# Kernel tuning notes

Measured on AMD Instinct MI355X. Metric: run time of the kernel, lower is better.

## Reference

```python
import jax, jax.numpy as jnp
import numpy as np

B, N, D, H = 2, 2048, 1024, 16
DH = D // H            # 64
PH = 3 * DH            # 192 per-head proj dim (module quirk: 3*Dh per head)
P = H * PH             # 3072 total projection width


def setup_inputs() -> dict:
    key = jax.random.key(0)
    ks = jax.random.split(key, 8)
    s = 0.02
    return {
        "input": jax.random.normal(ks[0], (B, N, D), dtype=jnp.float32),
        "q_w": jax.random.normal(ks[1], (D, P), dtype=jnp.float32) * s,
        "q_b": jnp.zeros((P,), dtype=jnp.float32),
        "k_w": jax.random.normal(ks[2], (D, P), dtype=jnp.float32) * s,
        "k_b": jnp.zeros((P,), dtype=jnp.float32),
        "v_w": jax.random.normal(ks[3], (D, P), dtype=jnp.float32) * s,
        "v_b": jnp.zeros((P,), dtype=jnp.float32),
        "o_w": jax.random.normal(ks[4], (P, D), dtype=jnp.float32) * s,
        "o_b": jnp.zeros((D,), dtype=jnp.float32),
    }


def reference(input, q_w, q_b, k_w, k_b, v_w, v_b, o_w, o_b):
    def heads(y):  # [B,N,H*PH] -> [B,H,N,PH]
        return y.reshape(B, N, H, PH).transpose(0, 2, 1, 3)

    q_mat = heads(input @ q_w + q_b)
    # faithful to source: v_mat uses the 'k' projection, k_mat uses the 'v' projection
    v_mat = heads(input @ k_w + k_b)
    k_mat = heads(input @ v_w + v_b)

    scale = 1.0 / jnp.sqrt(jnp.float32(DH * H))  # sqrt(dim), per source
    scores = jnp.einsum('bhnd,bhmd->bhnm', q_mat, k_mat) * scale
    weights = jax.nn.softmax(scores, axis=-1)
    inter = jnp.einsum('bhnm,bhmd->bhnd', weights, v_mat)
    inter = inter.transpose(0, 2, 1, 3).reshape(B, N, P)  # b n (h d)
    return inter @ o_w + o_b
```

## Files before the change

kernel.cpp:

```cpp
#include <hip/hip_runtime.h>
#include <cstdint>
#include <cstddef>

typedef __bf16 bf16;
typedef __attribute__((ext_vector_type(8))) __bf16 bf16x8;
typedef __attribute__((ext_vector_type(4))) __bf16 bf16x4;
typedef __attribute__((ext_vector_type(2))) __bf16 bf16x2;
typedef __attribute__((ext_vector_type(4))) float f32x4;

#define MFMA_16x16x32(a, b, c) __builtin_amdgcn_mfma_f32_16x16x32_bf16((a), (b), (c), 0, 0, 0)

#define VMCNT(N) asm volatile("s_waitcnt vmcnt(" #N ")" ::: "memory")
#define LGK0                                           \
  {                                                    \
    asm volatile("s_waitcnt lgkmcnt(0)" ::: "memory"); \
    __builtin_amdgcn_sched_barrier(0);                 \
  }

__device__ __forceinline__ void gload_lds16(const void* g, void* l) {
  __builtin_amdgcn_global_load_lds((__attribute__((address_space(1))) void*)g,
                                   (__attribute__((address_space(3))) void*)l,
                                   16, 0, 0);
}

__global__ __launch_bounds__(256) void prep_kernel(const float* __restrict__ X,
                                                   const float* __restrict__ q_w,
                                                   const float* __restrict__ v_w,
                                                   const float* __restrict__ k_w,
                                                   const float* __restrict__ o_w,
                                                   bf16* __restrict__ Xb,
                                                   bf16* __restrict__ Wqkv,
                                                   bf16* __restrict__ Wot) {
  __shared__ float tile[32][33];
  int blk = blockIdx.x;
  if (blk < 4096) {
    int i = blk * 256 + threadIdx.x;
    float4 v = ((const float4*)X)[i];
    bf16x4 o = {(bf16)v.x, (bf16)v.y, (bf16)v.z, (bf16)v.w};
    ((bf16x4*)Xb)[i] = o;
    return;
  }
  const float* in;
  bf16* out;
  int R, C, t;
  if (blk < 13312) {
    t = blk - 4096;
    int widx = t / 3072;
    t -= widx * 3072;
    in = widx == 0 ? q_w : (widx == 1 ? v_w : k_w);
    out = Wqkv + (size_t)widx * 3072 * 1024;
    R = 1024;
    C = 3072;
  } else {
    t = blk - 13312;
    in = o_w;
    out = Wot;
    R = 3072;
    C = 1024;
  }
  int tiles_c = C >> 5;
  int br = t / tiles_c, bc = t % tiles_c;
  int r0 = br << 5, c0 = bc << 5;
  int tr = threadIdx.x >> 5, tc = threadIdx.x & 31;
#pragma unroll
  for (int i = 0; i < 4; i++)
    tile[tr + 8 * i][tc] = in[(size_t)(r0 + tr + 8 * i) * C + c0 + tc];
  __syncthreads();
#pragma unroll
  for (int i = 0; i < 4; i++) {
    int oc = tr + 8 * i;
    out[(size_t)(c0 + oc) * R + r0 + tc] = (bf16)tile[tc][oc];
  }
}

__global__ __launch_bounds__(512, 2) void gemm_fused_qkv(
    const bf16* __restrict__ A, const bf16* __restrict__ Bt,
    const float* __restrict__ q_b, const float* __restrict__ v_b,
    const float* __restrict__ k_b,
    bf16* __restrict__ Qm, bf16* __restrict__ Km, bf16* __restrict__ Vt) {
  constexpr int K = 1024, NT = 16;
  __shared__ __align__(16) bf16 sA[2][2][128 * 32];
  __shared__ __align__(16) bf16 sB[2][192 * 64];

  int bid = blockIdx.x;
  int xcd = bid & 7, j = bid >> 3;
  int bm = xcd * 4 + (j & 3), bn = j >> 2;
  int m0 = bm << 7, n0 = bn * 192;

  int tid = threadIdx.x, lane = tid & 63, w = tid >> 6;
  int wr = w >> 2, wc = w & 3;
  int l15 = lane & 15, lg = lane >> 4;

  int sra = lane >> 2, sca = lane & 3;
  const bf16* gA = A + (size_t)(m0 + w * 16 + sra) * K + ((sca ^ ((sra >> 1) & 3)) * 8);
  int srb = lane >> 3, scb = lane & 7;
  const bf16* gB = Bt + (size_t)(n0 + w * 24 + srb) * K + ((scb ^ srb) * 8);

#define STAGE_AB(BUF, T)                                                   \
  {                                                                        \
    _Pragma("unroll") for (int kh = 0; kh < 2; kh++)                       \
        gload_lds16(gA + (size_t)(T) * 64 + kh * 32, &sA[BUF][kh][w * 512]); \
    _Pragma("unroll") for (int ii = 0; ii < 3; ii++)                       \
        gload_lds16(gB + (size_t)(ii * 8) * K + (T) * 64,                  \
                    &sB[BUF][(w * 3 + ii) * 512]);                         \
  }

  int slotA = lg ^ ((l15 >> 1) & 3);
  int aBase = wr * 2048 + l15 * 32 + slotA * 8;
  int bBase = (wc * 48 + l15) * 64;
  int sB0 = (lg ^ (l15 & 7)) * 8;
  int sB1 = ((4 + lg) ^ (l15 & 7)) * 8;

#define RD_A(BUF, KH)                                                      \
  _Pragma("unroll") for (int mf = 0; mf < 4; mf++)                         \
      a[mf] = *(const bf16x8*)&sA[BUF][KH][aBase + mf * 512];
#define RD_B(BUF, SLOT)                                                    \
  _Pragma("unroll") for (int nf = 0; nf < 3; nf++)                         \
      b[nf] = *(const bf16x8*)&sB[BUF][bBase + nf * 1024 + (SLOT)];
#define MFMA12                                                             \
  _Pragma("unroll") for (int mf = 0; mf < 4; mf++)                         \
      _Pragma("unroll") for (int nf = 0; nf < 3; nf++)                     \
          acc[mf][nf] = MFMA_16x16x32(a[mf], b[nf], acc[mf][nf]);

  f32x4 acc[4][3];
#pragma unroll
  for (int mf = 0; mf < 4; mf++)
#pragma unroll
    for (int nf = 0; nf < 3; nf++) acc[mf][nf] = (f32x4){0.f, 0.f, 0.f, 0.f};

  STAGE_AB(0, 0);

#pragma unroll 2
  for (int s = 0; s < NT; s++) {
    int buf = s & 1, nbuf = buf ^ 1;
    int nxt = (s + 1) & (NT - 1);
    bf16x8 a[4], b[3];

    STAGE_AB(nbuf, nxt);
    VMCNT(5);
    __builtin_amdgcn_s_barrier();

    RD_A(buf, 0);
    RD_B(buf, sB0);
    LGK0;
    __builtin_amdgcn_s_setprio(1);
    MFMA12;
    __builtin_amdgcn_s_setprio(0);

    RD_A(buf, 1);
    RD_B(buf, sB1);
    LGK0;
    __builtin_amdgcn_s_barrier();
    __builtin_amdgcn_s_setprio(1);
    MFMA12;
    __builtin_amdgcn_s_setprio(0);
  }

  int seg = bn >> 4;
  int segbn = bn & 15;
  const float* bias = seg == 0 ? q_b : (seg == 1 ? v_b : k_b);
  bf16* outQK = seg == 0 ? Qm : Km;
#pragma unroll
  for (int mf = 0; mf < 4; mf++) {
#pragma unroll
    for (int nf = 0; nf < 3; nf++) {
      int colL = segbn * 192 + wc * 48 + nf * 16 + l15;
      int row0 = m0 + wr * 64 + mf * 16 + lg * 4;
      float bv = bias[colL];
      if (seg < 2) {
#pragma unroll
        for (int r = 0; r < 4; r++)
          outQK[(size_t)(row0 + r) * 3072 + colL] = (bf16)(acc[mf][nf][r] + bv);
      } else {
        int hh = colL / 192, dd = colL % 192;
        int bi = row0 >> 11, nn = row0 & 2047;
        bf16x4 pk = {(bf16)(acc[mf][nf][0] + bv), (bf16)(acc[mf][nf][1] + bv),
                     (bf16)(acc[mf][nf][2] + bv), (bf16)(acc[mf][nf][3] + bv)};
        *(bf16x4*)(Vt + (((size_t)bi * 16 + hh) * 192 + dd) * 2048 + nn) = pk;
      }
    }
  }
#undef STAGE_AB
#undef RD_A
#undef RD_B
#undef MFMA12
}

__global__ __launch_bounds__(256, 3) void gemm_oproj(const bf16* __restrict__ A,
                                                     const bf16* __restrict__ Bt,
                                                     const float* __restrict__ bias,
                                                     float* __restrict__ out) {
  constexpr int K = 3072, NT = 48;
  __shared__ __align__(16) bf16 sA[2][2][128 * 32];
  __shared__ __align__(16) bf16 sB[2][2][64 * 32];

  int bid = blockIdx.x;
  int xcd = bid & 7, j = bid >> 3;
  int bm = xcd * 4 + (j & 3), bn = j >> 2;
  int m0 = bm << 7, n0 = bn << 6;

  int tid = threadIdx.x, lane = tid & 63, w = tid >> 6;
  int wr = w >> 1, wc = w & 1;
  int l15 = lane & 15, lg = lane >> 4;

  int sra = lane >> 2, sca = lane & 3;
  int swzS = (sca ^ ((sra >> 1) & 3)) * 8;
  const bf16* gA = A + (size_t)(m0 + w * 32 + sra) * K + swzS;
  const bf16* gB = Bt + (size_t)(n0 + w * 16 + sra) * K + swzS;

#define O_STAGE(BUF, T)                                                     \
  {                                                                         \
    _Pragma("unroll") for (int kh = 0; kh < 2; kh++) {                      \
      _Pragma("unroll") for (int ii = 0; ii < 2; ii++)                      \
          gload_lds16(gA + (size_t)(ii * 16) * K + (T) * 64 + kh * 32,      \
                      &sA[BUF][kh][(w * 32 + ii * 16) * 32]);               \
      gload_lds16(gB + (size_t)(T) * 64 + kh * 32, &sB[BUF][kh][w * 512]);  \
    }                                                                       \
  }

  int slotA = lg ^ ((l15 >> 1) & 3);
  int aBase = (wr * 64 + l15) * 32 + slotA * 8;
  int bBase = (wc * 32 + l15) * 32 + slotA * 8;

#define O_RD(BUF, KH)                                                      \
  {                                                                        \
    _Pragma("unroll") for (int mf = 0; mf < 4; mf++)                       \
        a[mf] = *(const bf16x8*)&sA[BUF][KH][aBase + mf * 512];             \
    _Pragma("unroll") for (int nf = 0; nf < 2; nf++)                       \
        b[nf] = *(const bf16x8*)&sB[BUF][KH][bBase + nf * 512];             \
  }
#define O_MFMA8                                                            \
  _Pragma("unroll") for (int mf = 0; mf < 4; mf++)                         \
      _Pragma("unroll") for (int nf = 0; nf < 2; nf++)                     \
          acc[mf][nf] = MFMA_16x16x32(a[mf], b[nf], acc[mf][nf]);

  f32x4 acc[4][2];
#pragma unroll
  for (int mf = 0; mf < 4; mf++)
#pragma unroll
    for (int nf = 0; nf < 2; nf++) acc[mf][nf] = (f32x4){0.f, 0.f, 0.f, 0.f};

  O_STAGE(0, 0);

#pragma unroll 2
  for (int s = 0; s < NT; s++) {
    int buf = s & 1, nbuf = buf ^ 1;
    int nxt = s + 1 < NT ? s + 1 : 0;
    bf16x8 a[4], b[2];

    O_STAGE(nbuf, nxt);
    VMCNT(6);
    __builtin_amdgcn_s_barrier();

    O_RD(buf, 0);
    LGK0;
    __builtin_amdgcn_s_setprio(1);
    O_MFMA8;
    __builtin_amdgcn_s_setprio(0);

    O_RD(buf, 1);
    LGK0;
    __builtin_amdgcn_s_barrier();
    __builtin_amdgcn_s_setprio(1);
    O_MFMA8;
    __builtin_amdgcn_s_setprio(0);
  }

#pragma unroll
  for (int mf = 0; mf < 4; mf++) {
#pragma unroll
    for (int nf = 0; nf < 2; nf++) {
      int col = n0 + wc * 32 + nf * 16 + l15;
      int row0 = m0 + wr * 64 + mf * 16 + lg * 4;
      float bv = bias[col];
#pragma unroll
      for (int r = 0; r < 4; r++)
        out[(size_t)(row0 + r) * 1024 + col] = acc[mf][nf][r] + bv;
    }
  }
#undef O_STAGE
#undef O_RD
#undef O_MFMA8
}

__global__ __launch_bounds__(512, 2) void attn_kernel(const bf16* __restrict__ Q,
                                                      const bf16* __restrict__ Km,
                                                      const bf16* __restrict__ Vt,
                                                      bf16* __restrict__ inter) {
  __shared__ __align__(16) bf16 sK[2][64 * 192];
  __shared__ __align__(16) bf16 sV[2][192 * 64];
  __shared__ __align__(16) bf16 sPT[8 * 2 * 16 * 72];

  int i = blockIdx.x;
  int j = i >> 3;
  int bh = (i & 7) * 4 + (j >> 3);
  int qt = j & 7;
  int b = bh >> 4, h = bh & 15;
  int tid = threadIdx.x, lane = tid & 63, w = tid >> 6;
  int l15 = lane & 15, lg = lane >> 4;
  int swz = l15 & 7;

  const bf16* Qh = Q + (size_t)b * 2048 * 3072 + (size_t)h * 192;
  const bf16* Kh = Km + (size_t)b * 2048 * 3072 + (size_t)h * 192;
  const bf16* Vh = Vt + (size_t)bh * 192 * 2048;

  int q0 = qt * 256 + w * 32;

  int kOff[3], vOff[3], ldsOff[3];
#pragma unroll
  for (int ii = 0; ii < 3; ii++) {
    int r = ii * 8 + w;
    int s = r * 64 + lane;
    int krow = s / 24, kc = s % 24;
    int kcs = (kc & 24) | ((kc & 7) ^ (krow & 7));
    kOff[ii] = krow * 3072 + kcs * 8;
    int vrow = s >> 3, vc = s & 7;
    int vcs = vc ^ (vrow & 7);
    vOff[ii] = vrow * 2048 + vcs * 8;
    ldsOff[ii] = r * 512;
  }

#define STAGE(BUF, KT)                                                      \
  {                                                                         \
    int kb = (KT) * 64;                                                     \
    _Pragma("unroll") for (int ii = 0; ii < 3; ii++) {                      \
      gload_lds16(Kh + (size_t)kb * 3072 + kOff[ii], &sK[BUF][ldsOff[ii]]); \
      gload_lds16(Vh + kb + vOff[ii], &sV[BUF][ldsOff[ii]]);                \
    }                                                                       \
  }

  STAGE(0, 0);

  bf16x8 aq[2][6];
#pragma unroll
  for (int rf = 0; rf < 2; rf++)
#pragma unroll
    for (int kc = 0; kc < 6; kc++)
      aq[rf][kc] = *(const bf16x8*)(Qh + (size_t)(q0 + rf * 16 + l15) * 3072 + kc * 32 + lg * 8);

  f32x4 o[2][12];
#pragma unroll
  for (int rf = 0; rf < 2; rf++)
#pragma unroll
    for (int df = 0; df < 12; df++) o[rf][df] = (f32x4){0.f, 0.f, 0.f, 0.f};
  float mrow[2] = {-1e30f, -1e30f};
  float lrow[2] = {0.f, 0.f};

  const float scl2 = 0.03125f * 1.44269504f;

  bf16* myPT0 = &sPT[((w * 2 + 0) * 16 + l15) * 72];
  bf16* myPT1 = &sPT[((w * 2 + 1) * 16 + l15) * 72];

  __syncthreads();

  for (int kt = 0; kt < 32; kt++) {
    const bf16* kbuf = sK[kt & 1];
    const bf16* vbuf = sV[kt & 1];
    if (kt < 31) STAGE((kt & 1) ^ 1, kt + 1);

    f32x4 st[4][2];
#pragma unroll
    for (int kf = 0; kf < 4; kf++)
#pragma unroll
      for (int rf = 0; rf < 2; rf++) st[kf][rf] = (f32x4){0.f, 0.f, 0.f, 0.f};
    __builtin_amdgcn_s_setprio(1);
#pragma unroll
    for (int kc = 0; kc < 6; kc++) {
      int g = kc * 4 + lg;
      int cc = (g & 24) | ((g & 7) ^ swz);
#pragma unroll
      for (int kf = 0; kf < 4; kf++) {
        bf16x8 bk = *(const bf16x8*)&kbuf[(kf * 16 + l15) * 192 + cc * 8];
        st[kf][0] = MFMA_16x16x32(bk, aq[0][kc], st[kf][0]);
        st[kf][1] = MFMA_16x16x32(bk, aq[1][kc], st[kf][1]);
      }
    }
    __builtin_amdgcn_s_setprio(0);

#pragma unroll
    for (int rf = 0; rf < 2; rf++) {
      bf16* myPT = rf ? myPT1 : myPT0;
      float mk[4];
#pragma unroll
      for (int kf = 0; kf < 4; kf++)
        mk[kf] = fmaxf(fmaxf(st[kf][rf][0], st[kf][rf][1]),
                       fmaxf(st[kf][rf][2], st[kf][rf][3]));
      float pmx = fmaxf(fmaxf(mk[0], mk[1]), fmaxf(mk[2], mk[3]));
      pmx = fmaxf(pmx, __shfl_xor(pmx, 16));
      pmx = fmaxf(pmx, __shfl_xor(pmx, 32));
      float pms = pmx * scl2;

      float mn = mrow[rf];
      if (!__all(pms - mn <= 11.0f)) {
        mn = fmaxf(mn, pms);
        float corr = exp2f(mrow[rf] - mn);
        mrow[rf] = mn;
        lrow[rf] *= corr;
#pragma unroll
        for (int df = 0; df < 12; df++) o[rf][df] *= corr;
      }

      float skf[4];
#pragma unroll
      for (int kf = 0; kf < 4; kf++) {
        float e0 = exp2f(fmaf(st[kf][rf][0], scl2, -mn));
        float e1 = exp2f(fmaf(st[kf][rf][1], scl2, -mn));
        float e2 = exp2f(fmaf(st[kf][rf][2], scl2, -mn));
        float e3 = exp2f(fmaf(st[kf][rf][3], scl2, -mn));
        skf[kf] = (e0 + e1) + (e2 + e3);
        bf16x4 pk4 = {(bf16)e0, (bf16)e1, (bf16)e2, (bf16)e3};
        *(bf16x4*)&myPT[kf * 16 + 4 * lg] = pk4;
      }
      float rs = (skf[0] + skf[1]) + (skf[2] + skf[3]);
      rs += __shfl_xor(rs, 16);
      rs += __shfl_xor(rs, 32);
      lrow[rf] += rs;
    }

    bf16x8 pf[2][2];
#pragma unroll
    for (int rf = 0; rf < 2; rf++) {
      bf16* myPT = rf ? myPT1 : myPT0;
#pragma unroll
      for (int ks = 0; ks < 2; ks++)
        pf[rf][ks] = *(const bf16x8*)&myPT[ks * 32 + lg * 8];
    }

    __builtin_amdgcn_s_setprio(1);
#pragma unroll
    for (int ks = 0; ks < 2; ks++) {
      int cv = (ks * 4 + lg) ^ swz;
#pragma unroll
      for (int df = 0; df < 12; df++) {
        bf16x8 av = *(const bf16x8*)&vbuf[(df * 16 + l15) * 64 + cv * 8];
        o[0][df] = MFMA_16x16x32(av, pf[0][ks], o[0][df]);
        o[1][df] = MFMA_16x16x32(av, pf[1][ks], o[1][df]);
      }
    }
    __builtin_amdgcn_s_setprio(0);

    __syncthreads();
  }

#pragma unroll
  for (int rf = 0; rf < 2; rf++) {
    float inv = 1.0f / lrow[rf];
    size_t token = (size_t)b * 2048 + q0 + rf * 16 + l15;
    bf16* outp = inter + token * 3072 + h * 192 + lg * 4;
#pragma unroll
    for (int df = 0; df < 12; df++) {
      bf16x4 pk = {(bf16)(o[rf][df][0] * inv), (bf16)(o[rf][df][1] * inv),
                   (bf16)(o[rf][df][2] * inv), (bf16)(o[rf][df][3] * inv)};
      *(bf16x4*)(outp + df * 16) = pk;
    }
  }
#undef STAGE
}

extern "C" void kernel_launch(void* const* d_in, const int* in_sizes, int n_in,
                              void* d_out, int out_size, void* d_ws, size_t ws_size,
                              hipStream_t stream) {
  const float* X = (const float*)d_in[0];
  const float* q_w = (const float*)d_in[1];
  const float* q_b = (const float*)d_in[2];
  const float* k_w = (const float*)d_in[3];
  const float* k_b = (const float*)d_in[4];
  const float* v_w = (const float*)d_in[5];
  const float* v_b = (const float*)d_in[6];
  const float* o_w = (const float*)d_in[7];
  const float* o_b = (const float*)d_in[8];

  char* ws = (char*)d_ws;
  bf16* Xb  = (bf16*)(ws);
  bf16* Wqt = (bf16*)(ws + 8388608);
  bf16* Wot = (bf16*)(ws + 27262976);
  bf16* Qm  = (bf16*)(ws + 33554432);
  bf16* Km  = (bf16*)(ws + 58720256);
  bf16* Vtw = (bf16*)(ws + 83886080);
  bf16* Im  = (bf16*)(ws + 109051904);

  prep_kernel<<<16384, 256, 0, stream>>>(X, q_w, v_w, k_w, o_w, Xb, Wqt, Wot);

  gemm_fused_qkv<<<1536, 512, 0, stream>>>(Xb, Wqt, q_b, v_b, k_b, Qm, Km, Vtw);

  attn_kernel<<<256, 512, 0, stream>>>(Qm, Km, Vtw, Im);

  gemm_oproj<<<512, 256, 0, stream>>>(Im, Wot, o_b, (float*)d_out);
}
```

Baseline: 273.4 us.

## Halve attention tile sizes to launch twice as many blocks

The attention kernel drops from 32 to 16 query rows per wave and from 64 to 32 keys per tile, and the grid doubles from 256 to 512 blocks. The aim is to fill all CUs on the device (256 blocks underfill it) and to cut per-wave registers and LDS. In exchange each K/V tile is reused by half as many queries, so K/V traffic and the number of barrier iterations double. The loader mapping and V swizzle are reworked for the narrower tiles.

```diff
diff --git a/kernel.cpp b/kernel.cpp
--- a/kernel.cpp
+++ b/kernel.cpp
@@ -287,14 +287,14 @@
                                                       const bf16* __restrict__ Km,
                                                       const bf16* __restrict__ Vt,
                                                       bf16* __restrict__ inter) {
-  __shared__ __align__(16) bf16 sK[2][64 * 192];
-  __shared__ __align__(16) bf16 sV[2][192 * 64];
-  __shared__ __align__(16) bf16 sPT[8 * 2 * 16 * 72];
+  __shared__ __align__(16) bf16 sK[2][32 * 192];
+  __shared__ __align__(16) bf16 sV[2][192 * 32];
+  __shared__ __align__(16) bf16 sPT[8 * 16 * 40];
 
   int i = blockIdx.x;
   int j = i >> 3;
-  int bh = (i & 7) * 4 + (j >> 3);
-  int qt = j & 7;
+  int bh = (i & 7) * 4 + (j >> 4);
+  int qt = j & 15;
   int b = bh >> 4, h = bh & 15;
   int tid = threadIdx.x, lane = tid & 63, w = tid >> 6;
   int l15 = lane & 15, lg = lane >> 4;
@@ -304,153 +304,134 @@
   const bf16* Kh = Km + (size_t)b * 2048 * 3072 + (size_t)h * 192;
   const bf16* Vh = Vt + (size_t)bh * 192 * 2048;
 
-  int q0 = qt * 256 + w * 32;
-
-  int kOff[3], vOff[3], ldsOff[3];
+  int q0 = qt * 128 + w * 16;
+
+  const bf16* gsrc[3];
+  int gstride[3];
+  bf16* lbase[3];
 #pragma unroll
   for (int ii = 0; ii < 3; ii++) {
-    int r = ii * 8 + w;
-    int s = r * 64 + lane;
-    int krow = s / 24, kc = s % 24;
-    int kcs = (kc & 24) | ((kc & 7) ^ (krow & 7));
-    kOff[ii] = krow * 3072 + kcs * 8;
-    int vrow = s >> 3, vc = s & 7;
-    int vcs = vc ^ (vrow & 7);
-    vOff[ii] = vrow * 2048 + vcs * 8;
-    ldsOff[ii] = r * 512;
+    int g = ii * 512 + tid;
+    if (g < 768) {
+      int krow = g / 24, kc = g % 24;
+      int kcs = (kc & 24) | ((kc & 7) ^ (krow & 7));
+      gsrc[ii] = Kh + krow * 3072 + kcs * 8;
+      gstride[ii] = 32 * 3072;
+      lbase[ii] = &sK[0][g * 8];
+    } else {
+      int gg = g - 768;
+      int vrow = gg >> 2, vc = gg & 3;
+      int vcs = vc ^ ((vrow >> 1) & 3);
+      gsrc[ii] = Vh + vrow * 2048 + vcs * 8;
+      gstride[ii] = 32;
+      lbase[ii] = &sV[0][gg * 8];
+    }
   }
 
 #define STAGE(BUF, KT)                                                      \
   {                                                                         \
-    int kb = (KT) * 64;                                                     \
-    _Pragma("unroll") for (int ii = 0; ii < 3; ii++) {                      \
-      gload_lds16(Kh + (size_t)kb * 3072 + kOff[ii], &sK[BUF][ldsOff[ii]]); \
-      gload_lds16(Vh + kb + vOff[ii], &sV[BUF][ldsOff[ii]]);                \
-    }                                                                       \
+    _Pragma("unroll") for (int ii = 0; ii < 3; ii++)                        \
+        gload_lds16(gsrc[ii] + (size_t)(KT) * gstride[ii],                  \
+                    lbase[ii] + (BUF) * 6144);                              \
   }
 
   STAGE(0, 0);
 
-  bf16x8 aq[2][6];
-#pragma unroll
-  for (int rf = 0; rf < 2; rf++)
-#pragma unroll
-    for (int kc = 0; kc < 6; kc++)
-      aq[rf][kc] = *(const bf16x8*)(Qh + (size_t)(q0 + rf * 16 + l15) * 3072 + kc * 32 + lg * 8);
-
-  f32x4 o[2][12];
-#pragma unroll
-  for (int rf = 0; rf < 2; rf++)
-#pragma unroll
-    for (int df = 0; df < 12; df++) o[rf][df] = (f32x4){0.f, 0.f, 0.f, 0.f};
-  float mrow[2] = {-1e30f, -1e30f};
-  float lrow[2] = {0.f, 0.f};
+  bf16x8 aq[6];
+#pragma unroll
+  for (int kc = 0; kc < 6; kc++)
+    aq[kc] = *(const bf16x8*)(Qh + (size_t)(q0 + l15) * 3072 + kc * 32 + lg * 8);
+
+  f32x4 o[12];
+#pragma unroll
+  for (int df = 0; df < 12; df++) o[df] = (f32x4){0.f, 0.f, 0.f, 0.f};
+  float mrow = -1e30f;
+  float lrow = 0.f;
 
   const float scl2 = 0.03125f * 1.44269504f;
 
-  bf16* myPT0 = &sPT[((w * 2 + 0) * 16 + l15) * 72];
-  bf16* myPT1 = &sPT[((w * 2 + 1) * 16 + l15) * 72];
+  bf16* myPT = &sPT[(w * 16 + l15) * 40];
+  int cv = lg ^ ((l15 >> 1) & 3);
 
   __syncthreads();
 
-  for (int kt = 0; kt < 32; kt++) {
+  for (int kt = 0; kt < 64; kt++) {
     const bf16* kbuf = sK[kt & 1];
     const bf16* vbuf = sV[kt & 1];
-    if (kt < 31) STAGE((kt & 1) ^ 1, kt + 1);
-
-    f32x4 st[4][2];
-#pragma unroll
-    for (int kf = 0; kf < 4; kf++)
-#pragma unroll
-      for (int rf = 0; rf < 2; rf++) st[kf][rf] = (f32x4){0.f, 0.f, 0.f, 0.f};
+    if (kt < 63) STAGE((kt & 1) ^ 1, kt + 1);
+
+    f32x4 st[2];
+    st[0] = (f32x4){0.f, 0.f, 0.f, 0.f};
+    st[1] = (f32x4){0.f, 0.f, 0.f, 0.f};
     __builtin_amdgcn_s_setprio(1);
 #pragma unroll
     for (int kc = 0; kc < 6; kc++) {
       int g = kc * 4 + lg;
       int cc = (g & 24) | ((g & 7) ^ swz);
 #pragma unroll
-      for (int kf = 0; kf < 4; kf++) {
+      for (int kf = 0; kf < 2; kf++) {
         bf16x8 bk = *(const bf16x8*)&kbuf[(kf * 16 + l15) * 192 + cc * 8];
-        st[kf][0] = MFMA_16x16x32(bk, aq[0][kc], st[kf][0]);
-        st[kf][1] = MFMA_16x16x32(bk, aq[1][kc], st[kf][1]);
+        st[kf] = MFMA_16x16x32(bk, aq[kc], st[kf]);
       }
     }
     __builtin_amdgcn_s_setprio(0);
 
-#pragma unroll
-    for (int rf = 0; rf < 2; rf++) {
-      bf16* myPT = rf ? myPT1 : myPT0;
-      float mk[4];
-#pragma unroll
-      for (int kf = 0; kf < 4; kf++)
-        mk[kf] = fmaxf(fmaxf(st[kf][rf][0], st[kf][rf][1]),
-                       fmaxf(st[kf][rf][2], st[kf][rf][3]));
-      float pmx = fmaxf(fmaxf(mk[0], mk[1]), fmaxf(mk[2], mk[3]));
+    {
+      float mk0 = fmaxf(fmaxf(st[0][0], st[0][1]), fmaxf(st[0][2], st[0][3]));
+      float mk1 = fmaxf(fmaxf(st[1][0], st[1][1]), fmaxf(st[1][2], st[1][3]));
+      float pmx = fmaxf(mk0, mk1);
       pmx = fmaxf(pmx, __shfl_xor(pmx, 16));
       pmx = fmaxf(pmx, __shfl_xor(pmx, 32));
       float pms = pmx * scl2;
 
-      float mn = mrow[rf];
+      float mn = mrow;
       if (!__all(pms - mn <= 11.0f)) {
         mn = fmaxf(mn, pms);
-        float corr = exp2f(mrow[rf] - mn);
-        mrow[rf] = mn;
-        lrow[rf] *= corr;
-#pragma unroll
-        for (int df = 0; df < 12; df++) o[rf][df] *= corr;
+        float corr = exp2f(mrow - mn);
+        mrow = mn;
+        lrow *= corr;
+#pragma unroll
+        for (int df = 0; df < 12; df++) o[df] *= corr;
       }
 
-      float skf[4];
-#pragma unroll
-      for (int kf = 0; kf < 4; kf++) {
-        float e0 = exp2f(fmaf(st[kf][rf][0], scl2, -mn));
-        float e1 = exp2f(fmaf(st[kf][rf][1], scl2, -mn));
-        float e2 = exp2f(fmaf(st[kf][rf][2], scl2, -mn));
-        float e3 = exp2f(fmaf(st[kf][rf][3], scl2, -mn));
+      float skf[2];
+#pragma unroll
+      for (int kf = 0; kf < 2; kf++) {
+        float e0 = exp2f(fmaf(st[kf][0], scl2, -mn));
+        float e1 = exp2f(fmaf(st[kf][1], scl2, -mn));
+        float e2 = exp2f(fmaf(st[kf][2], scl2, -mn));
+        float e3 = exp2f(fmaf(st[kf][3], scl2, -mn));
         skf[kf] = (e0 + e1) + (e2 + e3);
         bf16x4 pk4 = {(bf16)e0, (bf16)e1, (bf16)e2, (bf16)e3};
         *(bf16x4*)&myPT[kf * 16 + 4 * lg] = pk4;
       }
-      float rs = (skf[0] + skf[1]) + (skf[2] + skf[3]);
+      float rs = skf[0] + skf[1];
       rs += __shfl_xor(rs, 16);
       rs += __shfl_xor(rs, 32);
-      lrow[rf] += rs;
-    }
-
-    bf16x8 pf[2][2];
-#pragma unroll
-    for (int rf = 0; rf < 2; rf++) {
-      bf16* myPT = rf ? myPT1 : myPT0;
-#pragma unroll
-      for (int ks = 0; ks < 2; ks++)
-        pf[rf][ks] = *(const bf16x8*)&myPT[ks * 32 + lg * 8];
-    }
-
-    __builtin_amdgcn_s_setprio(1);
-#pragma unroll
-    for (int ks = 0; ks < 2; ks++) {
-      int cv = (ks * 4 + lg) ^ swz;
-#pragma unroll
-      for (int df = 0; df < 12; df++) {
-        bf16x8 av = *(const bf16x8*)&vbuf[(df * 16 + l15) * 64 + cv * 8];
-        o[0][df] = MFMA_16x16x32(av, pf[0][ks], o[0][df]);
-        o[1][df] = MFMA_16x16x32(av, pf[1][ks], o[1][df]);
-      }
+      lrow += rs;
+    }
+
+    bf16x8 pf = *(const bf16x8*)&myPT[lg * 8];
+
+    __builtin_amdgcn_s_setprio(1);
+#pragma unroll
+    for (int df = 0; df < 12; df++) {
+      bf16x8 av = *(const bf16x8*)&vbuf[(df * 16 + l15) * 32 + cv * 8];
+      o[df] = MFMA_16x16x32(av, pf, o[df]);
     }
     __builtin_amdgcn_s_setprio(0);
 
     __syncthreads();
   }
 
-#pragma unroll
-  for (int rf = 0; rf < 2; rf++) {
-    float inv = 1.0f / lrow[rf];
-    size_t token = (size_t)b * 2048 + q0 + rf * 16 + l15;
+  {
+    float inv = 1.0f / lrow;
+    size_t token = (size_t)b * 2048 + q0 + l15;
     bf16* outp = inter + token * 3072 + h * 192 + lg * 4;
 #pragma unroll
     for (int df = 0; df < 12; df++) {
-      bf16x4 pk = {(bf16)(o[rf][df][0] * inv), (bf16)(o[rf][df][1] * inv),
-                   (bf16)(o[rf][df][2] * inv), (bf16)(o[rf][df][3] * inv)};
+      bf16x4 pk = {(bf16)(o[df][0] * inv), (bf16)(o[df][1] * inv),
+                   (bf16)(o[df][2] * inv), (bf16)(o[df][3] * inv)};
       *(bf16x4*)(outp + df * 16) = pk;
     }
   }
@@ -483,7 +464,7 @@
 
   gemm_fused_qkv<<<1536, 512, 0, stream>>>(Xb, Wqt, q_b, v_b, k_b, Qm, Km, Vtw);
 
-  attn_kernel<<<256, 512, 0, stream>>>(Qm, Km, Vtw, Im);
+  attn_kernel<<<512, 512, 0, stream>>>(Qm, Km, Vtw, Im);
 
   gemm_oproj<<<512, 256, 0, stream>>>(Im, Wot, o_b, (float*)d_out);
 }
```

Result: no change. 271.3 us (-0.8%).
